# Optimization experiments

Hardware: AMD Instinct MI355X
Metric: run time of the kernel (lower is better)

Reference implementation:

```python
import jax, jax.numpy as jnp
import numpy as np

IN, OUT, BW = 2048, 2048, 8
L = 2 ** BW  # RNG sequence length
OFFSET = (2 * IN - 1) / 2.0  # module offset for non-scaled accumulation


def setup_inputs() -> dict:
    key = jax.random.key(0)
    ks = jax.random.split(key, 16)
    f = jnp.float32
    inp = {
        'input_r': jax.random.bernoulli(ks[0], 0.5, (1, IN)).astype(f),
        'input_i': jax.random.bernoulli(ks[1], 0.5, (1, IN)).astype(f),
        # SourceGen bipolar: round((w+1)/2 * 2^bw) in [0, 2^bw]
        'src_r': jax.random.randint(ks[2], (OUT, IN), 0, L + 1).astype(f),
        'src_i': jax.random.randint(ks[3], (OUT, IN), 0, L + 1).astype(f),
        # Sobol RNG of bitwidth 8 -> a permutation-like sequence of values 0..255
        'rng': jax.random.permutation(ks[4], L).astype(f),
    }
    names = ['idx1_fr_wr', 'idx0_fr_wr', 'idx1_fr_wi', 'idx0_fr_wi',
             'idx1_fi_wr', 'idx0_fi_wr', 'idx1_fi_wi', 'idx0_fi_wi']
    for i, n in enumerate(names):
        inp[n] = jax.random.randint(ks[5 + i], (OUT, IN), 0, L, dtype=jnp.int32)
    return inp


def _bit(src, rng, idx):
    # BSGen: bit = (source > rng[idx mod 2^bw])
    return (src > rng[idx % L]).astype(jnp.float32)


def _unary_kernel(x, src, rng, idx1, idx0):
    # kernel_1 weight = bit(src, idx1); kernel_0 weight = 1 - bit(src, idx0)
    w1 = _bit(src, rng, idx1)          # [O, I]
    w0 = 1.0 - _bit(src, rng, idx0)    # [O, I]
    # Linear(x) + Linear(1-x)  (no bias)
    return jnp.einsum('bi,oi->bo', x, w1) + jnp.einsum('bi,oi->bo', 1.0 - x, w0)


def reference(input_r, input_i, src_r, src_i, rng,
              idx1_fr_wr, idx0_fr_wr, idx1_fr_wi, idx0_fr_wi,
              idx1_fi_wr, idx0_fi_wr, idx1_fi_wi, idx0_fi_wi):
    o_fr_wr = _unary_kernel(input_r,       src_r, rng, idx1_fr_wr, idx0_fr_wr)
    o_fr_wi = _unary_kernel(input_r,       src_i, rng, idx1_fr_wi, idx0_fr_wi)
    o_fi_wr = _unary_kernel(input_i,       src_r, rng, idx1_fi_wr, idx0_fi_wr)
    o_fi_wi = _unary_kernel(1.0 - input_i, src_i, rng, idx1_fi_wi, idx0_fi_wi)
    # non-scaled accumulation (scaled=False), accumulators/out_accumulators start at 0
    acc_r = o_fr_wr + o_fi_wi - OFFSET
    out_r = (acc_r > 0.0).astype(jnp.float32)
    acc_i = o_fr_wi + o_fi_wr - OFFSET
    out_i = (acc_i > 0.0).astype(jnp.float32)
    return out_r, out_i
```

## Files before the change

kernel.cpp:

```cpp
#include <hip/hip_runtime.h>

#define IN_DIM 2048
#define OUT_DIM 2048

typedef __attribute__((ext_vector_type(4))) int int4v;

#define GLOAD(dst, ptr, voff)                                   \
    asm volatile("global_load_dwordx4 %0, %1, %2"               \
                 : "=v"(dst)                                    \
                 : "v"(voff), "s"(ptr)                          \
                 : "memory")

__global__ __launch_bounds__(256, 4) void ulc_kernel(
    const float* __restrict__ input_r, const float* __restrict__ input_i,
    const float* __restrict__ src_r,   const float* __restrict__ src_i,
    const float* __restrict__ rng,
    const int* __restrict__ i1_frwr, const int* __restrict__ i0_frwr,
    const int* __restrict__ i1_frwi, const int* __restrict__ i0_frwi,
    const int* __restrict__ i1_fiwr, const int* __restrict__ i0_fiwr,
    const int* __restrict__ i1_fiwi, const int* __restrict__ i0_fiwi,
    float* __restrict__ out)
{
    __shared__ float rng_s[256];
    __shared__ int redA[4], redB[4];
    const int tid = threadIdx.x;
    const int o = blockIdx.x;

    const float rv = rng[tid];
    const float4 xrA = *(const float4*)(input_r + tid * 4);
    const float4 xiA = *(const float4*)(input_i + tid * 4);
    const float4 xrB = *(const float4*)(input_r + 1024 + tid * 4);
    const float4 xiB = *(const float4*)(input_i + 1024 + tid * 4);
    rng_s[tid] = rv;

    const bool xr[8] = { xrA.x > 0.5f, xrA.y > 0.5f, xrA.z > 0.5f, xrA.w > 0.5f,
                         xrB.x > 0.5f, xrB.y > 0.5f, xrB.z > 0.5f, xrB.w > 0.5f };
    const bool xi[8] = { xiA.x > 0.5f, xiA.y > 0.5f, xiA.z > 0.5f, xiA.w > 0.5f,
                         xiB.x > 0.5f, xiB.y > 0.5f, xiB.z > 0.5f, xiB.w > 0.5f };
    __builtin_amdgcn_sched_barrier(0);

    const unsigned v0 = (unsigned)o * 8192u + (unsigned)tid * 16u;
    const unsigned v1 = v0 + 4096u;

    int4v sr0, si0, a1_0, a0_0, b1_0, b0_0, c1_0, c0_0, d1_0, d0_0;
    int4v sr1, si1, a1_1, a0_1, b1_1, b0_1, c1_1, c0_1, d1_1, d0_1;

    GLOAD(sr0, src_r,   v0);  GLOAD(si0, src_i,   v0);
    GLOAD(a1_0, i1_frwr, v0); GLOAD(a0_0, i0_frwr, v0);
    GLOAD(b1_0, i1_frwi, v0); GLOAD(b0_0, i0_frwi, v0);
    GLOAD(c1_0, i1_fiwr, v0); GLOAD(c0_0, i0_fiwr, v0);
    GLOAD(d1_0, i1_fiwi, v0); GLOAD(d0_0, i0_fiwi, v0);
    GLOAD(sr1, src_r,   v1);  GLOAD(si1, src_i,   v1);
    GLOAD(a1_1, i1_frwr, v1); GLOAD(a0_1, i0_frwr, v1);
    GLOAD(b1_1, i1_frwi, v1); GLOAD(b0_1, i0_frwi, v1);
    GLOAD(c1_1, i1_fiwr, v1); GLOAD(c0_1, i0_fiwr, v1);
    GLOAD(d1_1, i1_fiwi, v1); GLOAD(d0_1, i0_fiwi, v1);

    asm volatile("s_waitcnt lgkmcnt(0)" ::: "memory");
    __builtin_amdgcn_s_barrier();

    int accA = 0, accB = 0;

    #define ELEM(k, q, xq)                                                   \
    {                                                                        \
        const float sr = __int_as_float(sr##k[q]);                           \
        const float si = __int_as_float(si##k[q]);                           \
        const bool xr_ = xr[xq], xi_ = xi[xq];                               \
        const int ia = (xr_ ? a1_##k[q] : a0_##k[q]) & 255;                  \
        const int ib = (xr_ ? b1_##k[q] : b0_##k[q]) & 255;                  \
        const int ic = (xi_ ? c1_##k[q] : c0_##k[q]) & 255;                  \
        const int id = (xi_ ? d0_##k[q] : d1_##k[q]) & 255;                  \
        const bool cA = sr > rng_s[ia];                                      \
        const bool cB = si > rng_s[ib];                                      \
        const bool cC = sr > rng_s[ic];                                      \
        const bool cD = si > rng_s[id];                                      \
        accA += (int)(cA == xr_) + (int)(cD != xi_);                         \
        accB += (int)(cB == xr_) + (int)(cC == xi_);                         \
    }

    asm volatile("s_waitcnt vmcnt(10)" ::: "memory");
    __builtin_amdgcn_sched_barrier(0);
    ELEM(0, 0, 0) ELEM(0, 1, 1) ELEM(0, 2, 2) ELEM(0, 3, 3)

    asm volatile("s_waitcnt vmcnt(0)" ::: "memory");
    __builtin_amdgcn_sched_barrier(0);
    ELEM(1, 0, 4) ELEM(1, 1, 5) ELEM(1, 2, 6) ELEM(1, 3, 7)
    #undef ELEM

    #pragma unroll
    for (int off = 32; off > 0; off >>= 1) {
        accA += __shfl_down(accA, off);
        accB += __shfl_down(accB, off);
    }
    const int wid = tid >> 6;
    if ((tid & 63) == 0) { redA[wid] = accA; redB[wid] = accB; }
    __syncthreads();
    if (tid == 0) {
        const int sA = redA[0] + redA[1] + redA[2] + redA[3];
        const int sB = redB[0] + redB[1] + redB[2] + redB[3];
        out[o]           = (sA >= 2048) ? 1.0f : 0.0f;
        out[OUT_DIM + o] = (sB >= 2048) ? 1.0f : 0.0f;
    }
}

extern "C" void kernel_launch(void* const* d_in, const int* in_sizes, int n_in,
                              void* d_out, int out_size, void* d_ws, size_t ws_size,
                              hipStream_t stream) {
    const float* input_r = (const float*)d_in[0];
    const float* input_i = (const float*)d_in[1];
    const float* src_r   = (const float*)d_in[2];
    const float* src_i   = (const float*)d_in[3];
    const float* rng     = (const float*)d_in[4];
    const int* i1_frwr = (const int*)d_in[5];
    const int* i0_frwr = (const int*)d_in[6];
    const int* i1_frwi = (const int*)d_in[7];
    const int* i0_frwi = (const int*)d_in[8];
    const int* i1_fiwr = (const int*)d_in[9];
    const int* i0_fiwr = (const int*)d_in[10];
    const int* i1_fiwi = (const int*)d_in[11];
    const int* i0_fiwi = (const int*)d_in[12];
    float* out = (float*)d_out;

    ulc_kernel<<<dim3(OUT_DIM), dim3(256), 0, stream>>>(
        input_r, input_i, src_r, src_i, rng,
        i1_frwr, i0_frwr, i1_frwi, i0_frwi,
        i1_fiwr, i0_fiwr, i1_fiwi, i0_fiwi,
        out);
}
```

Baseline: 30.90 us.

## Process two rows per block with double-buffered software-pipelined loads

```diff
diff --git a/kernel.cpp b/kernel.cpp
--- a/kernel.cpp
+++ b/kernel.cpp
@@ -23,83 +23,109 @@
 {
     __shared__ float rng_s[256];
     __shared__ int redA[4], redB[4];
-    const int tid = threadIdx.x;
-    const int o = blockIdx.x;
+    const int tid  = threadIdx.x;
+    const int wid  = tid >> 6;
+    const int lane = tid & 63;
+    const int rowA = blockIdx.x * 2;
+    const int row  = rowA + (wid >> 1);
+    const int half = wid & 1;
 
     const float rv = rng[tid];
-    const float4 xrA = *(const float4*)(input_r + tid * 4);
-    const float4 xiA = *(const float4*)(input_i + tid * 4);
-    const float4 xrB = *(const float4*)(input_r + 1024 + tid * 4);
-    const float4 xiB = *(const float4*)(input_i + 1024 + tid * 4);
+    const int cbase = half * 1024 + lane * 4;
+    const float4 xr0 = *(const float4*)(input_r + cbase);
+    const float4 xr1 = *(const float4*)(input_r + cbase + 256);
+    const float4 xr2 = *(const float4*)(input_r + cbase + 512);
+    const float4 xr3 = *(const float4*)(input_r + cbase + 768);
+    const float4 xi0 = *(const float4*)(input_i + cbase);
+    const float4 xi1 = *(const float4*)(input_i + cbase + 256);
+    const float4 xi2 = *(const float4*)(input_i + cbase + 512);
+    const float4 xi3 = *(const float4*)(input_i + cbase + 768);
     rng_s[tid] = rv;
 
-    const bool xr[8] = { xrA.x > 0.5f, xrA.y > 0.5f, xrA.z > 0.5f, xrA.w > 0.5f,
-                         xrB.x > 0.5f, xrB.y > 0.5f, xrB.z > 0.5f, xrB.w > 0.5f };
-    const bool xi[8] = { xiA.x > 0.5f, xiA.y > 0.5f, xiA.z > 0.5f, xiA.w > 0.5f,
-                         xiB.x > 0.5f, xiB.y > 0.5f, xiB.z > 0.5f, xiB.w > 0.5f };
+    unsigned xrm = 0, xim = 0;
+    #define PACKB(k, xv, yv)                                                  \
+        xrm |= (((xv.x > 0.5f) ? 1u : 0u) << ((k)*4))                         \
+             | (((xv.y > 0.5f) ? 1u : 0u) << ((k)*4+1))                       \
+             | (((xv.z > 0.5f) ? 1u : 0u) << ((k)*4+2))                       \
+             | (((xv.w > 0.5f) ? 1u : 0u) << ((k)*4+3));                      \
+        xim |= (((yv.x > 0.5f) ? 1u : 0u) << ((k)*4))                         \
+             | (((yv.y > 0.5f) ? 1u : 0u) << ((k)*4+1))                       \
+             | (((yv.z > 0.5f) ? 1u : 0u) << ((k)*4+2))                       \
+             | (((yv.w > 0.5f) ? 1u : 0u) << ((k)*4+3));
+    PACKB(0, xr0, xi0) PACKB(1, xr1, xi1) PACKB(2, xr2, xi2) PACKB(3, xr3, xi3)
+    #undef PACKB
     __builtin_amdgcn_sched_barrier(0);
 
-    const unsigned v0 = (unsigned)o * 8192u + (unsigned)tid * 16u;
-    const unsigned v1 = v0 + 4096u;
+    const unsigned v0 = (unsigned)row * 8192u + (unsigned)half * 4096u
+                      + (unsigned)lane * 16u;
 
-    int4v sr0, si0, a1_0, a0_0, b1_0, b0_0, c1_0, c0_0, d1_0, d0_0;
-    int4v sr1, si1, a1_1, a0_1, b1_1, b0_1, c1_1, c0_1, d1_1, d0_1;
+    int4v srP, siP, a1P, a0P, b1P, b0P, c1P, c0P, d1P, d0P;
+    int4v srQ, siQ, a1Q, a0Q, b1Q, b0Q, c1Q, c0Q, d1Q, d0Q;
 
-    GLOAD(sr0, src_r,   v0);  GLOAD(si0, src_i,   v0);
-    GLOAD(a1_0, i1_frwr, v0); GLOAD(a0_0, i0_frwr, v0);
-    GLOAD(b1_0, i1_frwi, v0); GLOAD(b0_0, i0_frwi, v0);
-    GLOAD(c1_0, i1_fiwr, v0); GLOAD(c0_0, i0_fiwr, v0);
-    GLOAD(d1_0, i1_fiwi, v0); GLOAD(d0_0, i0_fiwi, v0);
-    GLOAD(sr1, src_r,   v1);  GLOAD(si1, src_i,   v1);
-    GLOAD(a1_1, i1_frwr, v1); GLOAD(a0_1, i0_frwr, v1);
-    GLOAD(b1_1, i1_frwi, v1); GLOAD(b0_1, i0_frwi, v1);
-    GLOAD(c1_1, i1_fiwr, v1); GLOAD(c0_1, i0_fiwr, v1);
-    GLOAD(d1_1, i1_fiwi, v1); GLOAD(d0_1, i0_fiwi, v1);
+    #define ISSUE(S, off)                                                     \
+        GLOAD(sr##S, src_r,   v0 + (off)); GLOAD(si##S, src_i,   v0 + (off)); \
+        GLOAD(a1##S, i1_frwr, v0 + (off)); GLOAD(a0##S, i0_frwr, v0 + (off)); \
+        GLOAD(b1##S, i1_frwi, v0 + (off)); GLOAD(b0##S, i0_frwi, v0 + (off)); \
+        GLOAD(c1##S, i1_fiwr, v0 + (off)); GLOAD(c0##S, i0_fiwr, v0 + (off)); \
+        GLOAD(d1##S, i1_fiwi, v0 + (off)); GLOAD(d0##S, i0_fiwi, v0 + (off));
+
+    ISSUE(P, 0u)
+    ISSUE(Q, 1024u)
 
     asm volatile("s_waitcnt lgkmcnt(0)" ::: "memory");
     __builtin_amdgcn_s_barrier();
 
     int accA = 0, accB = 0;
 
-    #define ELEM(k, q, xq)                                                   \
-    {                                                                        \
-        const float sr = __int_as_float(sr##k[q]);                           \
-        const float si = __int_as_float(si##k[q]);                           \
-        const bool xr_ = xr[xq], xi_ = xi[xq];                               \
-        const int ia = (xr_ ? a1_##k[q] : a0_##k[q]) & 255;                  \
-        const int ib = (xr_ ? b1_##k[q] : b0_##k[q]) & 255;                  \
-        const int ic = (xi_ ? c1_##k[q] : c0_##k[q]) & 255;                  \
-        const int id = (xi_ ? d0_##k[q] : d1_##k[q]) & 255;                  \
-        const bool cA = sr > rng_s[ia];                                      \
-        const bool cB = si > rng_s[ib];                                      \
-        const bool cC = sr > rng_s[ic];                                      \
-        const bool cD = si > rng_s[id];                                      \
-        accA += (int)(cA == xr_) + (int)(cD != xi_);                         \
-        accB += (int)(cB == xr_) + (int)(cC == xi_);                         \
+    #define ELEM(S, j, bit)                                                   \
+    {                                                                         \
+        const bool xr_ = (xrm >> (bit)) & 1u;                                 \
+        const bool xi_ = (xim >> (bit)) & 1u;                                 \
+        const float sr = __int_as_float(sr##S[j]);                            \
+        const float si = __int_as_float(si##S[j]);                            \
+        const int ia = (xr_ ? a1##S[j] : a0##S[j]) & 255;                     \
+        const int ib = (xr_ ? b1##S[j] : b0##S[j]) & 255;                     \
+        const int ic = (xi_ ? c1##S[j] : c0##S[j]) & 255;                     \
+        const int id = (xi_ ? d0##S[j] : d1##S[j]) & 255;                     \
+        const bool cA = sr > rng_s[ia];                                       \
+        const bool cB = si > rng_s[ib];                                       \
+        const bool cC = sr > rng_s[ic];                                       \
+        const bool cD = si > rng_s[id];                                       \
+        accA += (int)(cA == xr_) + (int)(cD != xi_);                          \
+        accB += (int)(cB == xr_) + (int)(cC == xi_);                          \
     }
+    #define BATCH(S, base) ELEM(S,0,(base)) ELEM(S,1,(base)+1) ELEM(S,2,(base)+2) ELEM(S,3,(base)+3)
 
     asm volatile("s_waitcnt vmcnt(10)" ::: "memory");
     __builtin_amdgcn_sched_barrier(0);
-    ELEM(0, 0, 0) ELEM(0, 1, 1) ELEM(0, 2, 2) ELEM(0, 3, 3)
-
+    BATCH(P, 0)
+    ISSUE(P, 2048u)
+    asm volatile("s_waitcnt vmcnt(10)" ::: "memory");
+    __builtin_amdgcn_sched_barrier(0);
+    BATCH(Q, 4)
+    ISSUE(Q, 3072u)
+    asm volatile("s_waitcnt vmcnt(10)" ::: "memory");
+    __builtin_amdgcn_sched_barrier(0);
+    BATCH(P, 8)
     asm volatile("s_waitcnt vmcnt(0)" ::: "memory");
     __builtin_amdgcn_sched_barrier(0);
-    ELEM(1, 0, 4) ELEM(1, 1, 5) ELEM(1, 2, 6) ELEM(1, 3, 7)
+    BATCH(Q, 12)
+    #undef BATCH
     #undef ELEM
+    #undef ISSUE
 
     #pragma unroll
     for (int off = 32; off > 0; off >>= 1) {
         accA += __shfl_down(accA, off);
         accB += __shfl_down(accB, off);
     }
-    const int wid = tid >> 6;
-    if ((tid & 63) == 0) { redA[wid] = accA; redB[wid] = accB; }
+    if (lane == 0) { redA[wid] = accA; redB[wid] = accB; }
     __syncthreads();
     if (tid == 0) {
-        const int sA = redA[0] + redA[1] + redA[2] + redA[3];
-        const int sB = redB[0] + redB[1] + redB[2] + redB[3];
-        out[o]           = (sA >= 2048) ? 1.0f : 0.0f;
-        out[OUT_DIM + o] = (sB >= 2048) ? 1.0f : 0.0f;
+        out[rowA]               = (redA[0] + redA[1] >= 2048) ? 1.0f : 0.0f;
+        out[rowA + 1]           = (redA[2] + redA[3] >= 2048) ? 1.0f : 0.0f;
+        out[OUT_DIM + rowA]     = (redB[0] + redB[1] >= 2048) ? 1.0f : 0.0f;
+        out[OUT_DIM + rowA + 1] = (redB[2] + redB[3] >= 2048) ? 1.0f : 0.0f;
     }
 }
 
@@ -121,7 +147,7 @@
     const int* i0_fiwi = (const int*)d_in[12];
     float* out = (float*)d_out;
 
-    ulc_kernel<<<dim3(OUT_DIM), dim3(256), 0, stream>>>(
+    ulc_kernel<<<dim3(OUT_DIM / 2), dim3(256), 0, stream>>>(
         input_r, input_i, src_r, src_i, rng,
         i1_frwr, i0_frwr, i1_frwi, i0_frwi,
         i1_fiwr, i0_fiwr, i1_fiwi, i0_fiwi,
```

Measured after the change: 29.97 us. 3.0% less time.
